# Performance work log

Hardware: AMD Instinct MI355X
Metric: run time of the kernel (lower is better)

The kernel has to match this reference:

```python
import jax, jax.numpy as jnp
import numpy as np

B, T, NH, NB = 16, 400, 100, 65
SR, BLOCK = 16000, 160
REV_LEN = SR  # Reverb(sampling_rate, sampling_rate)


def _fft_convolve(signal, kernel):
    # torch: pad signal right by n, kernel left by its length, multiply spectra, keep 2nd half
    n = signal.shape[-1]
    s = jnp.pad(signal, [(0, 0)] * (signal.ndim - 1) + [(0, n)])
    k = jnp.pad(kernel, [(0, 0)] * (kernel.ndim - 1) + [(kernel.shape[-1], 0)])
    out = jnp.fft.irfft(jnp.fft.rfft(s) * jnp.fft.rfft(k), s.shape[-1])
    return out[..., out.shape[-1] // 2:]


def _amp_to_impulse_response(amp, target_size):
    # amp: [..., n_bands] real magnitudes treated as zero-phase rfft coefficients
    ir = jnp.fft.irfft(jax.lax.complex(amp, jnp.zeros_like(amp)))  # [..., 2*(NB-1)]
    fs = ir.shape[-1]
    ir = jnp.roll(ir, fs // 2, axis=-1)
    win = 0.5 - 0.5 * jnp.cos(2.0 * np.pi * jnp.arange(fs, dtype=ir.dtype) / fs)  # periodic hann
    ir = ir * win
    ir = jnp.pad(ir, [(0, 0)] * (ir.ndim - 1) + [(0, target_size - fs)])
    return jnp.roll(ir, -fs // 2, axis=-1)


def setup_inputs() -> dict:
    key = jax.random.key(0)
    ks = jax.random.split(key, 6)
    pitch = 40.0 + 400.0 * jax.random.uniform(ks[0], (B, T, 1), dtype=jnp.float32)
    total_amp = jax.random.uniform(ks[1], (B, T), dtype=jnp.float32)
    harmo_amps = jax.random.uniform(ks[2], (B, NH, T), dtype=jnp.float32) + 1e-3
    noise_filter = 0.1 * jax.random.uniform(ks[3], (B, T, NB), dtype=jnp.float32)
    noise = 2.0 * jax.random.uniform(ks[4], (B, T, BLOCK), dtype=jnp.float32) - 1.0
    reverb_noise = 2.0 * jax.random.uniform(ks[5], (REV_LEN, 1), dtype=jnp.float32) - 1.0
    decay = jnp.asarray(5.0, jnp.float32)
    wet = jnp.asarray(0.0, jnp.float32)
    return dict(pitch=pitch, total_amp=total_amp, harmo_amps=harmo_amps,
                noise_filter=noise_filter, noise=noise, reverb_noise=reverb_noise,
                decay=decay, wet=wet, sampling_rate=SR, block_size=BLOCK)


def reference(pitch, total_amp, harmo_amps, noise_filter, noise, reverb_noise,
              decay, wet, sampling_rate, block_size):
    dt = pitch.dtype
    n_harm = harmo_amps.shape[1]
    harm_idx = jnp.arange(1, n_harm + 1, dtype=dt)
    # remove_above_nyquist: mask harmonics whose freq >= sr/2 (tiny epsilon kept, as in DDSP)
    freqs = pitch[:, :, 0][:, None, :] * harm_idx[None, :, None]          # [B,NH,T]
    aa = (freqs < (sampling_rate / 2)).astype(dt) + 1e-4
    amps = harmo_amps * aa
    amps = jnp.transpose(amps, (0, 2, 1))                                  # [B,T,NH]
    amps = amps / jnp.sum(amps, axis=-1, keepdims=True)
    amps = amps * total_amp[..., None]
    # nearest-neighbor upsample by block_size (F.interpolate default mode)
    amps_up = jnp.repeat(amps, block_size, axis=1)                         # [B,N,NH]
    pitch_up = jnp.repeat(pitch, block_size, axis=1)                       # [B,N,1]
    # harmonic additive synthesis
    omega = jnp.cumsum(2.0 * np.pi * pitch_up / sampling_rate, axis=1)     # [B,N,1]
    harmonic = jnp.sum(jnp.sin(omega * harm_idx) * amps_up, axis=-1, keepdims=True)
    # filtered noise branch
    impulse = _amp_to_impulse_response(noise_filter, block_size)           # [B,T,BLOCK]
    noise_f = _fft_convolve(noise, impulse)                                # [B,T,BLOCK]
    noise_f = noise_f.reshape(noise_f.shape[0], -1, 1)                     # [B,N,1]
    signal = harmonic + noise_f
    # reverb (forward with reverb=True)
    rev_len = reverb_noise.shape[0]
    t = (jnp.arange(rev_len, dtype=dt) / sampling_rate)[None, :, None]     # [1,L,1]
    imp = reverb_noise[None] * jnp.exp(-jax.nn.softplus(-decay) * t * 500.0) * jax.nn.sigmoid(wet)
    imp = imp.at[:, 0].set(1.0)
    imp = jnp.pad(imp, ((0, 0), (0, signal.shape[1] - rev_len), (0, 0)))   # [1,N,1]
    out = _fft_convolve(signal[..., 0], imp[..., 0])[..., None]            # [B,N,1]
    return out
```

## Files before the change

### kernel.cpp

```cpp
#include <hip/hip_runtime.h>

#define B_ 16
#define T_ 400
#define NH_ 100
#define NB_ 65
#define BLK_ 160
#define SR_ 16000
#define N_ 64000
#define REV_ 16000
#define KPAD_ 16128
#define KTOT_ 80128
#define M_ 16
#define NWG_ 250
#define ISTRIDE_ 16768

typedef __attribute__((ext_vector_type(8))) _Float16 f16x8;
typedef __attribute__((ext_vector_type(2))) _Float16 f16x2;
typedef __attribute__((ext_vector_type(4))) float f32x4;

static __device__ __forceinline__ float dot2f(f16x2 a, f16x2 b, float c) {
#if __has_builtin(__builtin_amdgcn_fdot2)
  return __builtin_amdgcn_fdot2(a, b, c, false);
#else
  return fmaf((float)a[0], (float)b[0], fmaf((float)a[1], (float)b[1], c));
#endif
}

__global__ __launch_bounds__(512) void k_pre(const float* __restrict__ pitch,
                                             const float* __restrict__ rn,
                                             const float* __restrict__ dec,
                                             const float* __restrict__ wet,
                                             double* __restrict__ Pv,
                                             double* __restrict__ Xv,
                                             _Float16* __restrict__ IMPREV,
                                             _Float16* __restrict__ PH) {
  const int blk = blockIdx.x, tid = threadIdx.x;
  if (blk < 66) {
    const int gid = blk * 512 + tid;
    if (gid < 2 * ISTRIDE_) {
      const int c = gid / ISTRIDE_, u = gid - c * ISTRIDE_;
      const int i = 16383 - u - c;
      float v = 0.f;
      if (i == 0) {
        v = 1.0f;
      } else if (i > 0 && i < REV_) {
        const float a = log1pf(expf(-dec[0]));
        const float sg = 1.f / (1.f + expf(-wet[0]));
        v = rn[i] * expf(-a * ((float)i / (float)SR_) * 500.0f) * sg;
      }
      IMPREV[gid] = (_Float16)v;
    }
    return;
  }
  if (blk < 129) {
    const int gid = (blk - 66) * 512 + tid;
    ((f32x4*)PH)[gid] = (f32x4){0.f, 0.f, 0.f, 0.f};
    return;
  }
  __shared__ double s[512];
  const int b = blk - 129, t = tid;
  double x = 0.0;
  if (t < T_) x = (double)pitch[b * T_ + t] * (1.0 / (double)SR_);
  s[t] = x;
  __syncthreads();
  for (int off = 1; off < 512; off <<= 1) {
    double v = (t >= off) ? s[t - off] : 0.0;
    __syncthreads();
    s[t] += v;
    __syncthreads();
  }
  if (t < T_) {
    Xv[b * T_ + t] = x;
    Pv[b * T_ + t] = (s[t] - x) * 160.0;
  }
}

__global__ __launch_bounds__(320) void k_synth(
    const float* __restrict__ pitch, const float* __restrict__ tamp,
    const float* __restrict__ harmo, const float* __restrict__ nfilt,
    const float* __restrict__ noise, const double* __restrict__ Pv,
    const double* __restrict__ Xv, _Float16* __restrict__ PH) {
  const int tid = threadIdx.x;
  const int g = (tid >= 160) ? 1 : 0;
  const int ltid = tid - (g << 7) - (g << 5);
  const int bt = (blockIdx.x << 1) + g;
  const int b = bt / T_, t = bt - b * T_;
  __shared__ __align__(16) float amp[2][112];
  __shared__ __align__(16) float a_s[2][68];
  __shared__ __align__(16) float ir_s[2][68];
  __shared__ __align__(16) _Float16 C0[2][320];
  __shared__ __align__(16) _Float16 C1[2][320];
  __shared__ __align__(16) _Float16 imp_sw[2][128];
  __shared__ float red_s[2];

  const float pv = pitch[bt];
  int nv = (int)(8000.0f / pv);
  if (nv > NH_) nv = NH_;
  while (nv < NH_ && (float)(nv + 1) * pv < 8000.0f) ++nv;
  while (nv > 0 && (float)nv * pv >= 8000.0f) --nv;

  if (ltid < NB_) a_s[g][ltid] = nfilt[bt * NB_ + ltid];
  {
    const _Float16 nh = (_Float16)noise[bt * BLK_ + ltid];
    C0[g][160 + ltid] = nh;
    C1[g][159 + ltid] = nh;
    C0[g][ltid] = (_Float16)0.f;
    if (ltid < 159) C1[g][ltid] = (_Float16)0.f;
  }
  if (ltid < NH_) {
    const float ha = harmo[(b * NH_ + ltid) * T_ + t];
    const float aa = (pv * (float)(ltid + 1) < 8000.0f ? 1.0f : 0.0f) + 1e-4f;
    amp[g][ltid] = ha * aa;
  } else if (ltid < 112) {
    amp[g][ltid] = 0.f;
  }
  __syncthreads();

  float irv = 0.f;
  if (ltid < 65) {
    const float phi = (float)ltid * (1.0f / 128.0f);
    const float c1 = __builtin_amdgcn_cosf(phi);
    const float c2 = fmaf(2.f * c1, c1, -1.f);
    const float c3 = fmaf(2.f * c2, c1, -c1);
    const float c4 = fmaf(2.f * c2, c2, -1.f);
    const float tc = 2.f * c4;
    float x0 = 1.f, p0 = c4;
    float x1 = c1, p1 = c3;
    float x2 = c2, p2 = c2;
    float x3 = c3, p3 = c1;
    float a0 = 0.f, a1 = 0.f, a2 = 0.f, a3 = 0.f;
#pragma unroll
    for (int m = 0; m < 8; ++m) {
      const f32x4 aA = *(const f32x4*)&a_s[g][m << 3];
      const f32x4 aB = *(const f32x4*)&a_s[g][(m << 3) + 4];
      a0 = fmaf(aA[0], x0, a0); const float y0 = fmaf(tc, x0, -p0);
      a1 = fmaf(aA[1], x1, a1); const float y1 = fmaf(tc, x1, -p1);
      a2 = fmaf(aA[2], x2, a2); const float y2 = fmaf(tc, x2, -p2);
      a3 = fmaf(aA[3], x3, a3); const float y3 = fmaf(tc, x3, -p3);
      a0 = fmaf(aB[0], y0, a0); const float z0 = fmaf(tc, y0, -x0); p0 = y0; x0 = z0;
      a1 = fmaf(aB[1], y1, a1); const float z1 = fmaf(tc, y1, -x1); p1 = y1; x1 = z1;
      a2 = fmaf(aB[2], y2, a2); const float z2 = fmaf(tc, y2, -x2); p2 = y2; x2 = z2;
      a3 = fmaf(aB[3], y3, a3); const float z3 = fmaf(tc, y3, -x3); p3 = y3; x3 = z3;
    }
    const float accS = (a0 + a1) + (a2 + a3);
    irv = (2.f * accS - a_s[g][0] + ((ltid & 1) ? -a_s[g][64] : a_s[g][64])) * (1.0f / 128.0f);
    ir_s[g][ltid] = irv;
  } else if (ltid >= 128) {
    const int l = ltid - 128;
    float v = amp[g][l] + amp[g][l + 32] + amp[g][l + 64] + (l < 4 ? amp[g][l + 96] : 0.f);
    v += __shfl_xor(v, 16);
    v += __shfl_xor(v, 8);
    v += __shfl_xor(v, 4);
    v += __shfl_xor(v, 2);
    v += __shfl_xor(v, 1);
    if (l == 0) red_s[g] = v;
  }
  __syncthreads();

  if (ltid < 64) {
    const float w = 0.5f + 0.5f * __builtin_amdgcn_cosf((float)ltid * (1.0f / 128.0f));
    imp_sw[g][ltid ^ 1] = (_Float16)(w * irv);
  } else if (ltid >= 96 && ltid < 160) {
    const int u = ltid - 96;
    const float w = 0.5f - 0.5f * __builtin_amdgcn_cosf((float)u * (1.0f / 128.0f));
    imp_sw[g][64 + (u ^ 1)] = (_Float16)(w * ir_s[g][64 - u]);
  }
  const float scale = tamp[bt] / red_s[g];
  double th = Pv[bt] + (double)(ltid + 1) * Xv[bt];
  th -= floor(th);
  const float theta = (float)th;
  const float cT = __builtin_amdgcn_cosf(theta);
  const float sT = __builtin_amdgcn_sinf(theta);
  __syncthreads();

  float acc;
  {
    const float c2 = fmaf(cT, cT, -sT * sT);
    const float s2 = 2.f * cT * sT;
    const float s3 = fmaf(s2, cT, c2 * sT);
    const float s4 = 2.f * s2 * c2;
    const float c4 = fmaf(2.f * c2, c2, -1.f);
    const float tc = 2.f * c4;
    float x0 = sT, p0 = -s3;
    float x1 = s2, p1 = -s2;
    float x2 = s3, p2 = -sT;
    float x3 = s4, p3 = 0.f;
    float a0 = 0.f, a1 = 0.f, a2 = 0.f, a3 = 0.f;
    const int S = (nv + 7) >> 3;
    for (int m = 0; m < S; ++m) {
      const f32x4 aA = *(const f32x4*)&amp[g][m << 3];
      const f32x4 aB = *(const f32x4*)&amp[g][(m << 3) + 4];
      a0 = fmaf(aA[0], x0, a0); const float y0 = fmaf(tc, x0, -p0);
      a1 = fmaf(aA[1], x1, a1); const float y1 = fmaf(tc, x1, -p1);
      a2 = fmaf(aA[2], x2, a2); const float y2 = fmaf(tc, x2, -p2);
      a3 = fmaf(aA[3], x3, a3); const float y3 = fmaf(tc, x3, -p3);
      a0 = fmaf(aB[0], y0, a0); const float z0 = fmaf(tc, y0, -x0); p0 = y0; x0 = z0;
      a1 = fmaf(aB[1], y1, a1); const float z1 = fmaf(tc, y1, -x1); p1 = y1; x1 = z1;
      a2 = fmaf(aB[2], y2, a2); const float z2 = fmaf(tc, y2, -x2); p2 = y2; x2 = z2;
      a3 = fmaf(aB[3], y3, a3); const float z3 = fmaf(tc, y3, -x3); p3 = y3; x3 = z3;
    }
    acc = ((a0 + a1) + (a2 + a3)) * scale;
  }

  float nf = 0.f;
  {
    const f16x2* np0;
    int pe;
    if (ltid & 1) {
      np0 = (const f16x2*)C0[g];
      pe = (159 + ltid) >> 1;
    } else {
      np0 = (const f16x2*)C1[g];
      pe = (158 + ltid) >> 1;
    }
    const f16x8* ip = (const f16x8*)imp_sw[g];
#pragma unroll
    for (int k0 = 0; k0 < 8; ++k0) {
      const f16x8 i8 = ip[k0];
      const int kb = k0 << 2;
      nf = dot2f((f16x2){i8[0], i8[1]}, np0[pe - kb], nf);
      nf = dot2f((f16x2){i8[2], i8[3]}, np0[pe - kb - 1], nf);
      nf = dot2f((f16x2){i8[4], i8[5]}, np0[pe - kb - 2], nf);
      nf = dot2f((f16x2){i8[6], i8[7]}, np0[pe - kb - 3], nf);
    }
#pragma unroll
    for (int k0 = 0; k0 < 8; ++k0) {
      const f16x8 i8 = ip[8 + k0];
      const int kb = (k0 << 2) + 48;
      nf = dot2f((f16x2){i8[0], i8[1]}, np0[pe - kb], nf);
      nf = dot2f((f16x2){i8[2], i8[3]}, np0[pe - kb - 1], nf);
      nf = dot2f((f16x2){i8[4], i8[5]}, np0[pe - kb - 2], nf);
      nf = dot2f((f16x2){i8[6], i8[7]}, np0[pe - kb - 3], nf);
    }
  }

  const float v = acc + nf;
  const unsigned k = (unsigned)(KPAD_ + t * BLK_ + ltid);
  const unsigned off = ((k >> 3) << 7) + ((unsigned)b << 3) + (k & 7u);
  PH[off] = (_Float16)v;
}

static __device__ __forceinline__ f32x4 mfma_f16(f16x8 a, f16x8 b, f32x4 c) {
  return __builtin_amdgcn_mfma_f32_16x16x32_f16(a, b, c, 0, 0, 0);
}

static __device__ __forceinline__ f16x8 lfrag(const unsigned short* __restrict__ base, int byteoff) {
  const unsigned* p = (const unsigned*)((const char*)base + byteoff);
  union { unsigned u[4]; f16x8 v; } x;
  x.u[0] = p[0]; x.u[1] = p[1]; x.u[2] = p[2]; x.u[3] = p[3];
  return x.v;
}

template <int U, bool ISSUE, bool CONSUME>
__device__ __forceinline__ void conv_step(f16x8 (&Rh)[M_], f32x4 (&acc)[M_], f16x8 (&bhi2)[2],
                                          f16x8 (&nb)[2], f16x8 (&na0)[2], f16x8 (&na1)[2],
                                          const f16x8* __restrict__ ph,
                                          const unsigned short* __restrict__ abase,
                                          int& kit, int& abyte) {
  if (ISSUE) {
    kit += 64;
    nb[U & 1] = ph[kit];
    abyte += 64;
    na0[U & 1] = lfrag(abase, abyte);
    na1[U & 1] = lfrag(abase, abyte - 32);
  }
#pragma unroll
  for (int mm = 0; mm < M_; ++mm) {
    const int m = (mm + M_ - 2) & (M_ - 1);
    const int sl = (m - 2 * U) & (M_ - 1);
    acc[m] = mfma_f16(Rh[sl], bhi2[U & 1], acc[m]);
  }
  if (CONSUME) {
    Rh[(M_ - 2 - 2 * U) & (M_ - 1)] = na0[(U + 1) & 1];
    Rh[(M_ - 1 - 2 * U) & (M_ - 1)] = na1[(U + 1) & 1];
    bhi2[(U + 1) & 1] = nb[(U + 1) & 1];
  }
}

__global__ __launch_bounds__(512) void k_mconv(const unsigned short* __restrict__ IMPREV,
                                               const f16x8* __restrict__ PH,
                                               float* __restrict__ out) {
  const int tid = threadIdx.x;
  const int s = tid >> 6, lane = tid & 63;
  int w = blockIdx.x;
  {
    const int q = NWG_ / 8, r = NWG_ % 8;
    const int xcd = w & 7, o = w >> 3;
    w = (xcd < r ? xcd * (q + 1) : r * (q + 1) + (xcd - r) * q) + o;
  }
  const int Q0 = w << 8;
  const int T0 = 1022 - 128 * s;

  const int pat = (lane & 15) - ((lane >> 4) << 3);
  const int o0 = 16223 - 16 * T0 - pat;
  const int par = o0 & 1;
  const unsigned short* abase = IMPREV + (par ? ISTRIDE_ : 0);
  int abyte = 2 * (384 + o0 - par);

  f16x8 Rh[M_];
#pragma unroll
  for (int m = 0; m < M_; ++m) Rh[m] = lfrag(abase, abyte - 32 * m);
  f32x4 acc[M_];
#pragma unroll
  for (int m = 0; m < M_; ++m) acc[m] = (f32x4){0.f, 0.f, 0.f, 0.f};

  const f16x8* ph = PH + ((lane >> 4) << 4) + (lane & 15);
  int kit = (Q0 + 2048 * s) << 1;
  f16x8 bhi2[2], nb[2], na0[2], na1[2];
  bhi2[0] = ph[kit];
  kit += 64;
  nb[1] = ph[kit];
  abyte += 64;
  na0[1] = lfrag(abase, abyte);
  na1[1] = lfrag(abase, abyte - 32);

  for (int ii = 0; ii < 7; ++ii) {
    conv_step<0, true, true>(Rh, acc, bhi2, nb, na0, na1, ph, abase, kit, abyte);
    conv_step<1, true, true>(Rh, acc, bhi2, nb, na0, na1, ph, abase, kit, abyte);
    conv_step<2, true, true>(Rh, acc, bhi2, nb, na0, na1, ph, abase, kit, abyte);
    conv_step<3, true, true>(Rh, acc, bhi2, nb, na0, na1, ph, abase, kit, abyte);
    conv_step<4, true, true>(Rh, acc, bhi2, nb, na0, na1, ph, abase, kit, abyte);
    conv_step<5, true, true>(Rh, acc, bhi2, nb, na0, na1, ph, abase, kit, abyte);
    conv_step<6, true, true>(Rh, acc, bhi2, nb, na0, na1, ph, abase, kit, abyte);
    conv_step<7, true, true>(Rh, acc, bhi2, nb, na0, na1, ph, abase, kit, abyte);
  }
  conv_step<0, true, true>(Rh, acc, bhi2, nb, na0, na1, ph, abase, kit, abyte);
  conv_step<1, true, true>(Rh, acc, bhi2, nb, na0, na1, ph, abase, kit, abyte);
  conv_step<2, true, true>(Rh, acc, bhi2, nb, na0, na1, ph, abase, kit, abyte);
  conv_step<3, true, true>(Rh, acc, bhi2, nb, na0, na1, ph, abase, kit, abyte);
  conv_step<4, true, true>(Rh, acc, bhi2, nb, na0, na1, ph, abase, kit, abyte);
  conv_step<5, true, true>(Rh, acc, bhi2, nb, na0, na1, ph, abase, kit, abyte);
  conv_step<6, false, true>(Rh, acc, bhi2, nb, na0, na1, ph, abase, kit, abyte);
  conv_step<7, false, false>(Rh, acc, bhi2, nb, na0, na1, ph, abase, kit, abyte);

  __shared__ f32x4 part[4][M_][64];
  if (s < 4) {
#pragma unroll
    for (int m = 0; m < M_; ++m) part[s][m][lane] = acc[m];
  }
  __syncthreads();
  if (s >= 4) {
#pragma unroll
    for (int m = 0; m < M_; ++m) part[s - 4][m][lane] += acc[m];
  }
  __syncthreads();
#pragma unroll
  for (int half = 0; half < 2; ++half) {
    const int it = tid + (half << 9);
    const int m = it >> 6, ln = it & 63;
    f32x4 v = part[0][m][ln];
    v += part[1][m][ln];
    v += part[2][m][ln];
    v += part[3][m][ln];
    const int b = ln & 15, gq = ln >> 4;
    *(f32x4*)(out + (size_t)b * N_ + Q0 + (m << 4) + (gq << 2)) = v;
  }
}

extern "C" void kernel_launch(void* const* d_in, const int* in_sizes, int n_in,
                              void* d_out, int out_size, void* d_ws, size_t ws_size,
                              hipStream_t stream) {
  const float* pitch = (const float*)d_in[0];
  const float* tamp  = (const float*)d_in[1];
  const float* harmo = (const float*)d_in[2];
  const float* nfilt = (const float*)d_in[3];
  const float* noise = (const float*)d_in[4];
  const float* rn    = (const float*)d_in[5];
  const float* dec   = (const float*)d_in[6];
  const float* wet   = (const float*)d_in[7];

  char* ws = (char*)d_ws;
  size_t off = 0;
  _Float16* PH = (_Float16*)(ws + off);     off += (size_t)KTOT_ * 16 * 2;
  _Float16* IMPREV = (_Float16*)(ws + off); off += (size_t)2 * ISTRIDE_ * 2;
  double* Pv = (double*)(ws + off);         off += (size_t)B_ * T_ * 8;
  double* Xv = (double*)(ws + off);         off += (size_t)B_ * T_ * 8;
  float* out = (float*)d_out;

  k_pre<<<dim3(145), dim3(512), 0, stream>>>(pitch, rn, dec, wet, Pv, Xv, IMPREV, PH);
  k_synth<<<dim3(B_ * T_ / 2), dim3(320), 0, stream>>>(pitch, tamp, harmo, nfilt, noise, Pv, Xv, PH);
  k_mconv<<<dim3(NWG_), dim3(512), 0, stream>>>((const unsigned short*)IMPREV, (const f16x8*)PH, out);
}
```

Before: 58.89 us.

## Halve conv output tile per workgroup, double grid, simplify prefetch pipeline

The MFMA reverb convolution now computes 128 outputs per workgroup instead of 256 (M_ 16→8), doubling the grid to 500 workgroups and re-deriving the per-wave K ranges. The double-buffered register prefetch is collapsed to a single-step prefetch, fragment loads become one vector load, and launch bounds request higher occupancy. The intent is to cut register pressure and improve load balance and latency hiding across CUs, at the cost of reloading more of the impulse per output and doing more partial-sum reduction per workgroup.

```diff
diff --git a/kernel.cpp b/kernel.cpp
--- a/kernel.cpp
+++ b/kernel.cpp
@@ -10,13 +10,15 @@
 #define REV_ 16000
 #define KPAD_ 16128
 #define KTOT_ 80128
-#define M_ 16
-#define NWG_ 250
+#define M_ 8
+#define NWG_ 500
 #define ISTRIDE_ 16768
 
 typedef __attribute__((ext_vector_type(8))) _Float16 f16x8;
 typedef __attribute__((ext_vector_type(2))) _Float16 f16x2;
 typedef __attribute__((ext_vector_type(4))) float f32x4;
+typedef __attribute__((ext_vector_type(4))) unsigned uint4v;
+typedef uint4v __attribute__((aligned(4))) uint4v_a4;
 
 static __device__ __forceinline__ float dot2f(f16x2 a, f16x2 b, float c) {
 #if __has_builtin(__builtin_amdgcn_fdot2)
@@ -245,41 +247,40 @@
 }
 
 static __device__ __forceinline__ f16x8 lfrag(const unsigned short* __restrict__ base, int byteoff) {
-  const unsigned* p = (const unsigned*)((const char*)base + byteoff);
-  union { unsigned u[4]; f16x8 v; } x;
-  x.u[0] = p[0]; x.u[1] = p[1]; x.u[2] = p[2]; x.u[3] = p[3];
+  union { uint4v u; f16x8 v; } x;
+  x.u = *(const uint4v_a4*)((const char*)base + byteoff);
   return x.v;
 }
 
-template <int U, bool ISSUE, bool CONSUME>
-__device__ __forceinline__ void conv_step(f16x8 (&Rh)[M_], f32x4 (&acc)[M_], f16x8 (&bhi2)[2],
-                                          f16x8 (&nb)[2], f16x8 (&na0)[2], f16x8 (&na1)[2],
+template <int U, bool PF>
+__device__ __forceinline__ void conv_step(f16x8 (&Rh)[M_], f32x4 (&acc)[M_], f16x8& bhi,
                                           const f16x8* __restrict__ ph,
                                           const unsigned short* __restrict__ abase,
                                           int& kit, int& abyte) {
-  if (ISSUE) {
+  f16x8 nbh, na0, na1;
+  if (PF) {
     kit += 64;
-    nb[U & 1] = ph[kit];
+    nbh = ph[kit];
     abyte += 64;
-    na0[U & 1] = lfrag(abase, abyte);
-    na1[U & 1] = lfrag(abase, abyte - 32);
+    na0 = lfrag(abase, abyte);
+    na1 = lfrag(abase, abyte - 32);
   }
 #pragma unroll
   for (int mm = 0; mm < M_; ++mm) {
     const int m = (mm + M_ - 2) & (M_ - 1);
     const int sl = (m - 2 * U) & (M_ - 1);
-    acc[m] = mfma_f16(Rh[sl], bhi2[U & 1], acc[m]);
-  }
-  if (CONSUME) {
-    Rh[(M_ - 2 - 2 * U) & (M_ - 1)] = na0[(U + 1) & 1];
-    Rh[(M_ - 1 - 2 * U) & (M_ - 1)] = na1[(U + 1) & 1];
-    bhi2[(U + 1) & 1] = nb[(U + 1) & 1];
-  }
-}
-
-__global__ __launch_bounds__(512) void k_mconv(const unsigned short* __restrict__ IMPREV,
-                                               const f16x8* __restrict__ PH,
-                                               float* __restrict__ out) {
+    acc[m] = mfma_f16(Rh[sl], bhi, acc[m]);
+  }
+  if (PF) {
+    Rh[(M_ - 2 - 2 * U) & (M_ - 1)] = na0;
+    Rh[(M_ - 1 - 2 * U) & (M_ - 1)] = na1;
+    bhi = nbh;
+  }
+}
+
+__global__ __launch_bounds__(512, 4) void k_mconv(const unsigned short* __restrict__ IMPREV,
+                                                  const f16x8* __restrict__ PH,
+                                                  float* __restrict__ out) {
   const int tid = threadIdx.x;
   const int s = tid >> 6, lane = tid & 63;
   int w = blockIdx.x;
@@ -288,8 +289,8 @@
     const int xcd = w & 7, o = w >> 3;
     w = (xcd < r ? xcd * (q + 1) : r * (q + 1) + (xcd - r) * q) + o;
   }
-  const int Q0 = w << 8;
-  const int T0 = 1022 - 128 * s;
+  const int Q0 = w << 7;
+  const int T0 = 1014 - 126 * s;
 
   const int pat = (lane & 15) - ((lane >> 4) << 3);
   const int o0 = 16223 - 16 * T0 - pat;
@@ -305,33 +306,18 @@
   for (int m = 0; m < M_; ++m) acc[m] = (f32x4){0.f, 0.f, 0.f, 0.f};
 
   const f16x8* ph = PH + ((lane >> 4) << 4) + (lane & 15);
-  int kit = (Q0 + 2048 * s) << 1;
-  f16x8 bhi2[2], nb[2], na0[2], na1[2];
-  bhi2[0] = ph[kit];
-  kit += 64;
-  nb[1] = ph[kit];
-  abyte += 64;
-  na0[1] = lfrag(abase, abyte);
-  na1[1] = lfrag(abase, abyte - 32);
-
-  for (int ii = 0; ii < 7; ++ii) {
-    conv_step<0, true, true>(Rh, acc, bhi2, nb, na0, na1, ph, abase, kit, abyte);
-    conv_step<1, true, true>(Rh, acc, bhi2, nb, na0, na1, ph, abase, kit, abyte);
-    conv_step<2, true, true>(Rh, acc, bhi2, nb, na0, na1, ph, abase, kit, abyte);
-    conv_step<3, true, true>(Rh, acc, bhi2, nb, na0, na1, ph, abase, kit, abyte);
-    conv_step<4, true, true>(Rh, acc, bhi2, nb, na0, na1, ph, abase, kit, abyte);
-    conv_step<5, true, true>(Rh, acc, bhi2, nb, na0, na1, ph, abase, kit, abyte);
-    conv_step<6, true, true>(Rh, acc, bhi2, nb, na0, na1, ph, abase, kit, abyte);
-    conv_step<7, true, true>(Rh, acc, bhi2, nb, na0, na1, ph, abase, kit, abyte);
-  }
-  conv_step<0, true, true>(Rh, acc, bhi2, nb, na0, na1, ph, abase, kit, abyte);
-  conv_step<1, true, true>(Rh, acc, bhi2, nb, na0, na1, ph, abase, kit, abyte);
-  conv_step<2, true, true>(Rh, acc, bhi2, nb, na0, na1, ph, abase, kit, abyte);
-  conv_step<3, true, true>(Rh, acc, bhi2, nb, na0, na1, ph, abase, kit, abyte);
-  conv_step<4, true, true>(Rh, acc, bhi2, nb, na0, na1, ph, abase, kit, abyte);
-  conv_step<5, true, true>(Rh, acc, bhi2, nb, na0, na1, ph, abase, kit, abyte);
-  conv_step<6, false, true>(Rh, acc, bhi2, nb, na0, na1, ph, abase, kit, abyte);
-  conv_step<7, false, false>(Rh, acc, bhi2, nb, na0, na1, ph, abase, kit, abyte);
+  int kit = (Q0 + 128 + 2016 * s) << 1;
+  f16x8 bhi = ph[kit];
+
+  for (int ii = 0; ii < 15; ++ii) {
+    conv_step<0, true>(Rh, acc, bhi, ph, abase, kit, abyte);
+    conv_step<1, true>(Rh, acc, bhi, ph, abase, kit, abyte);
+    conv_step<2, true>(Rh, acc, bhi, ph, abase, kit, abyte);
+    conv_step<3, true>(Rh, acc, bhi, ph, abase, kit, abyte);
+  }
+  conv_step<0, true>(Rh, acc, bhi, ph, abase, kit, abyte);
+  conv_step<1, true>(Rh, acc, bhi, ph, abase, kit, abyte);
+  conv_step<2, false>(Rh, acc, bhi, ph, abase, kit, abyte);
 
   __shared__ f32x4 part[4][M_][64];
   if (s < 4) {
@@ -344,10 +330,8 @@
     for (int m = 0; m < M_; ++m) part[s - 4][m][lane] += acc[m];
   }
   __syncthreads();
-#pragma unroll
-  for (int half = 0; half < 2; ++half) {
-    const int it = tid + (half << 9);
-    const int m = it >> 6, ln = it & 63;
+  {
+    const int m = tid >> 6, ln = tid & 63;
     f32x4 v = part[0][m][ln];
     v += part[1][m][ln];
     v += part[2][m][ln];
```

Result: slower. 69.69 us (+18.3%).
